# Performance work log

Measured on AMD Instinct MI355X. Metric: run time of the kernel, lower is better.

The kernel has to match this reference:

```python
import jax, jax.numpy as jnp
import numpy as np

HIDDEN = 1024
INNER = 2048  # hidden * expand_factor
STATE = 64
K = 4  # conv kernel size
BATCH, SEQ = 2, 2048


def setup_inputs() -> dict:
    key = jax.random.key(0)
    ks = jax.random.split(key, 8)
    def w(k, shape, scale=0.02):
        return (jax.random.normal(k, shape, jnp.float32) * scale)
    return {
        "x": jax.random.normal(ks[0], (BATCH, SEQ, HIDDEN), jnp.float32),
        "W_in": w(ks[1], (HIDDEN, 2 * INNER)),
        "conv_w": w(ks[2], (INNER, 1, K), 0.2),   # depthwise conv kernel [O, I/groups=1, K]
        "conv_b": jnp.zeros((INNER,), jnp.float32),
        "W_dt": w(ks[3], (INNER, INNER)),
        "b_dt": jnp.linspace(-4.0, -2.0, INNER).astype(jnp.float32),  # log(exp(linspace)) = linspace
        "W_B": w(ks[4], (INNER, STATE)),
        "W_C": w(ks[5], (INNER, STATE)),
        "D": jnp.ones((INNER,), jnp.float32),
        "W_out": w(ks[6], (INNER, HIDDEN)),
    }


def reference(x, W_in, conv_w, conv_b, W_dt, b_dt, W_B, W_C, D, W_out):
    batch, seq_len, _ = x.shape
    inner = W_dt.shape[0]
    state_dim = W_B.shape[1]

    # input projection and gate split
    xz = x @ W_in                              # [B, L, 2*inner]
    x_inner, z = jnp.split(xz, 2, axis=-1)

    # causal depthwise conv1d (pad both sides by K-1 then truncate == left-pad K-1)
    xc = jnp.transpose(x_inner, (0, 2, 1))    # [B, inner, L]
    k = conv_w.shape[-1]
    xc = jax.lax.conv_general_dilated(
        xc, conv_w, window_strides=(1,), padding=[(k - 1, 0)],
        dimension_numbers=("NCH", "OIH", "NCH"), feature_group_count=inner)
    xc = xc + conv_b[None, :, None]
    xc = jax.nn.silu(jnp.transpose(xc, (0, 2, 1)))   # [B, L, inner]

    # selective SSM parameters
    dt = jax.nn.softplus(xc @ W_dt + b_dt)    # [B, L, inner]
    Bm = xc @ W_B                             # [B, L, N]
    Cm = xc @ W_C                             # [B, L, N]
    a = jnp.exp(-dt)                          # [B, L, inner]
    dtx = dt * xc                             # [B, L, inner]

    # sequential selective scan over time: state[B, inner, N]
    def step(state, inp):
        a_t, dtx_t, b_t, c_t = inp
        state = a_t[..., None] * state + dtx_t[..., None] * b_t[:, None, :]
        y_t = jnp.einsum("bin,bn->bi", state, c_t)
        return state, y_t

    init = jnp.zeros((batch, inner, state_dim), x.dtype)
    xs = (jnp.swapaxes(a, 0, 1), jnp.swapaxes(dtx, 0, 1),
          jnp.swapaxes(Bm, 0, 1), jnp.swapaxes(Cm, 0, 1))
    _, ys = jax.lax.scan(step, init, xs)      # ys: [L, B, inner]
    y = jnp.swapaxes(ys, 0, 1) + D * xc       # skip connection

    y = y * jax.nn.silu(z)                    # output gate
    return y @ W_out                          # [B, L, hidden]
```

## Files before the change

### kernel.cpp

```cpp
#include <hip/hip_runtime.h>
#include <hip/hip_bf16.h>
#include <math.h>

#define BATCH  2
#define SEQ    2048
#define HID    1024
#define INNER  2048
#define NSTATE 64
#define NTOK   (BATCH * SEQ)
#define TCHUNK 64
#define NCHUNK (SEQ / TCHUNK)
#define NMID   (INNER + 2 * NSTATE)
#define LDH    1056
#define LDI    2080

typedef __bf16 bf16x8 __attribute__((ext_vector_type(8)));
typedef float  f32x4  __attribute__((ext_vector_type(4)));

typedef const __attribute__((address_space(1))) char* gas_ptr;
typedef __attribute__((address_space(3))) char*       las_ptr;

__device__ __forceinline__ void gload16(const void* g, void* l) {
  __builtin_amdgcn_global_load_lds((gas_ptr)g, (las_ptr)l, 16, 0, 0);
}

__device__ __forceinline__ unsigned short f2bf(float f) {
  __hip_bfloat16 h = __float2bfloat16(f);
  return __builtin_bit_cast(unsigned short, h);
}
__device__ __forceinline__ float bf2f(unsigned short u) {
  unsigned int x = ((unsigned int)u) << 16;
  return __builtin_bit_cast(float, x);
}

__global__ __launch_bounds__(256) void cvt_pad_kernel(
    const float* __restrict__ in, __hip_bfloat16* __restrict__ out, int n4) {
  int i = blockIdx.x * 256 + threadIdx.x;
  if (i >= n4) return;
  const int r = i >> 8;
  const int c = (i & 255) * 4;
  float4 v = *(const float4*)&in[(size_t)r * HID + c];
  ushort4 u;
  u.x = f2bf(v.x); u.y = f2bf(v.y); u.z = f2bf(v.z); u.w = f2bf(v.w);
  *(ushort4*)&out[(size_t)r * LDH + c] = u;
}

__global__ __launch_bounds__(256) void transpose_cvt_kernel(
    const float* __restrict__ in, __hip_bfloat16* __restrict__ out,
    int R, int C, int ostride) {
  __shared__ float tile[32][33];
  int tx = threadIdx.x & 31, ty = threadIdx.x >> 5;
  int c0 = blockIdx.x * 32, r0 = blockIdx.y * 32;
#pragma unroll
  for (int i = 0; i < 4; ++i)
    tile[ty + 8 * i][tx] = in[(size_t)(r0 + ty + 8 * i) * C + c0 + tx];
  __syncthreads();
#pragma unroll
  for (int i = 0; i < 4; ++i)
    out[(size_t)(c0 + ty + 8 * i) * ostride + r0 + tx] =
        __float2bfloat16(tile[tx][ty + 8 * i]);
}

template <int EPI>
__global__ __launch_bounds__(256, 4) void gemm_bt_kernel(
    const __hip_bfloat16* __restrict__ A, const __hip_bfloat16* __restrict__ Bt,
    int M, int N, int Klen, int ldk, int gridN, int nwg, int mnwg,
    float* __restrict__ Cout, int ldc, int ldo,
    __hip_bfloat16* __restrict__ o0, __hip_bfloat16* __restrict__ o1) {
  __shared__ __align__(16) __hip_bfloat16 As[128 * 64];
  __shared__ __align__(16) __hip_bfloat16 Bs[128 * 64];
  const int tid = threadIdx.x;
  const int lane = tid & 63;
  const int w = tid >> 6;
  const int wr = w >> 1, wc = w & 1;

  const int orig = blockIdx.x;
  const int q8 = nwg >> 3, r8 = nwg & 7;
  const int xcd = orig & 7, seq = orig >> 3;
  const int wg = (xcd < r8 ? xcd * (q8 + 1) : r8 * (q8 + 1) + (xcd - r8) * q8) + seq;
  const int kz = wg / mnwg;
  const int wgr = wg - kz * mnwg;
  const int m0 = (wgr / gridN) * 128;
  const int n0 = (wgr % gridN) * 128;

  const __hip_bfloat16* Ab = A + (size_t)kz * Klen;
  const __hip_bfloat16* Bb = Bt + (size_t)kz * Klen;

  f32x4 acc[4][4];
#pragma unroll
  for (int i = 0; i < 4; ++i)
#pragma unroll
    for (int j = 0; j < 4; ++j)
#pragma unroll
      for (int r2 = 0; r2 < 4; ++r2) acc[i][j][r2] = 0.f;

  const int g8row = lane >> 3;
  const int scol = ((lane & 7) ^ g8row) * 8;
  const __hip_bfloat16* Agp = Ab + (size_t)(m0 + w * 32 + g8row) * ldk + scol;
  const __hip_bfloat16* Bgp = Bb + (size_t)(n0 + w * 32 + g8row) * ldk + scol;
  __hip_bfloat16* lA = As + (w * 32) * 64;
  __hip_bfloat16* lB = Bs + (w * 32) * 64;

  const int lrow = lane & 15, lk = lane >> 4;
  const int arow0 = wr * 64 + lrow;
  const int brow0 = wc * 64 + lrow;

  const int nt = Klen >> 6;
  for (int t = 0; t < nt; ++t) {
    __syncthreads();
#pragma unroll
    for (int g = 0; g < 4; ++g) {
      gload16(Agp + (size_t)(g * 8) * ldk + t * 64, lA + (g * 8) * 64);
      gload16(Bgp + (size_t)(g * 8) * ldk + t * 64, lB + (g * 8) * 64);
    }
    __syncthreads();
#pragma unroll
    for (int ss = 0; ss < 2; ++ss) {
      bf16x8 af[4], bv[4];
#pragma unroll
      for (int i = 0; i < 4; ++i) {
        const int ra = arow0 + i * 16;
        af[i] = *(const bf16x8*)(As + ra * 64 + (((ss * 4 + lk) ^ (ra & 7)) * 8));
        const int rb = brow0 + i * 16;
        bv[i] = *(const bf16x8*)(Bs + rb * 64 + (((ss * 4 + lk) ^ (rb & 7)) * 8));
      }
#pragma unroll
      for (int i = 0; i < 4; ++i)
#pragma unroll
        for (int j = 0; j < 4; ++j)
          acc[i][j] = __builtin_amdgcn_mfma_f32_16x16x32_bf16(af[i], bv[j], acc[i][j], 0, 0, 0);
    }
  }

#pragma unroll
  for (int i = 0; i < 4; ++i) {
#pragma unroll
    for (int j = 0; j < 4; ++j) {
#pragma unroll
      for (int r2 = 0; r2 < 4; ++r2) {
        const int row = m0 + wr * 64 + i * 16 + lk * 4 + r2;
        const int col = n0 + wc * 64 + j * 16 + lrow;
        const float v = acc[i][j][r2];
        if constexpr (EPI == 0) {
          Cout[(size_t)kz * M * ldc + (size_t)row * ldc + col] = v;
        } else if constexpr (EPI == 1) {
          if (col < INNER) o0[(size_t)row * ldo + col] = __float2bfloat16(v);
          else             o1[(size_t)row * ldo + (col - INNER)] = __float2bfloat16(v);
        } else {
          o0[(size_t)kz * M * ldc + (size_t)row * ldc + col] = __float2bfloat16(v);
        }
      }
    }
  }
}

__global__ __launch_bounds__(256) void reduce4b_kernel(
    const __hip_bfloat16* __restrict__ P, float* __restrict__ out, int n4) {
  int i = blockIdx.x * 256 + threadIdx.x;
  if (i >= n4) return;
  float4 acc = make_float4(0.f, 0.f, 0.f, 0.f);
#pragma unroll
  for (int pp = 0; pp < 4; ++pp) {
    ushort4 u = ((const ushort4*)P)[(size_t)pp * n4 + i];
    acc.x += bf2f(u.x); acc.y += bf2f(u.y); acc.z += bf2f(u.z); acc.w += bf2f(u.w);
  }
  ((float4*)out)[i] = acc;
}

__global__ __launch_bounds__(256) void conv_silu_kernel(
    const __hip_bfloat16* __restrict__ xin, const float* __restrict__ cw,
    const float* __restrict__ cb, __hip_bfloat16* __restrict__ xch) {
  int idx = blockIdx.x * 256 + threadIdx.x;
  int cg = idx & 511;
  int tok = idx >> 9;
  int c = cg * 4;
  int l = tok & (SEQ - 1);
  float wv[4][4];
#pragma unroll
  for (int i = 0; i < 4; ++i) {
    float4 w = *(const float4*)&cw[(c + i) * 4];
    wv[i][0] = w.x; wv[i][1] = w.y; wv[i][2] = w.z; wv[i][3] = w.w;
  }
  float4 bias = *(const float4*)&cb[c];
  float r0 = bias.x, r1 = bias.y, r2 = bias.z, r3 = bias.w;
#pragma unroll
  for (int k = 0; k < 4; ++k) {
    const int d = 3 - k;
    if (l >= d) {
      ushort4 xv = *(const ushort4*)&xin[(size_t)(tok - d) * LDI + c];
      r0 = fmaf(bf2f(xv.x), wv[0][k], r0);
      r1 = fmaf(bf2f(xv.y), wv[1][k], r1);
      r2 = fmaf(bf2f(xv.z), wv[2][k], r2);
      r3 = fmaf(bf2f(xv.w), wv[3][k], r3);
    }
  }
  r0 = r0 / (1.f + __expf(-r0));
  r1 = r1 / (1.f + __expf(-r1));
  r2 = r2 / (1.f + __expf(-r2));
  r3 = r3 / (1.f + __expf(-r3));
  ushort4 u;
  u.x = f2bf(r0); u.y = f2bf(r1); u.z = f2bf(r2); u.w = f2bf(r3);
  *(ushort4*)&xch[(size_t)tok * LDI + c] = u;
}

__global__ __launch_bounds__(256) void cumv_kernel(
    const __hip_bfloat16* __restrict__ P, const float* __restrict__ bdt,
    const __hip_bfloat16* __restrict__ xch,
    unsigned short* __restrict__ cumA, unsigned int* __restrict__ wT) {
  __shared__ float dpre[64][68];
  __shared__ float xcs[64][68];
  const int bk = blockIdx.y;
  const int c0 = blockIdx.x * 64;
  const int b = bk >> 5, k = bk & 31;
  const size_t tokbase = (size_t)(b * SEQ + k * TCHUNK);
  const unsigned short* P0 = (const unsigned short*)P;
  const unsigned short* P1 = P0 + (size_t)NTOK * NMID;
  const unsigned short* XC = (const unsigned short*)xch;

  const int g = threadIdx.x & 15;
  const int r0 = threadIdx.x >> 4;
  const float4 bias4 = *(const float4*)&bdt[c0 + g * 4];
#pragma unroll
  for (int rr = 0; rr < 4; ++rr) {
    const int row = r0 + rr * 16;
    const size_t tok = tokbase + row;
    ushort4 u0 = *(const ushort4*)&P0[tok * NMID + c0 + g * 4];
    ushort4 u1 = *(const ushort4*)&P1[tok * NMID + c0 + g * 4];
    ushort4 ux = *(const ushort4*)&XC[tok * LDI + c0 + g * 4];
    float4 d = make_float4(bf2f(u0.x) + bf2f(u1.x) + bias4.x,
                           bf2f(u0.y) + bf2f(u1.y) + bias4.y,
                           bf2f(u0.z) + bf2f(u1.z) + bias4.z,
                           bf2f(u0.w) + bf2f(u1.w) + bias4.w);
    *(float4*)&dpre[row][g * 4] = d;
    *(float4*)&xcs[row][g * 4] = make_float4(bf2f(ux.x), bf2f(ux.y), bf2f(ux.z), bf2f(ux.w));
  }
  __syncthreads();

  const int cl = threadIdx.x >> 2, h = threadIdx.x & 3;
  const int c = c0 + cl;
  float dt[16], lc[16];
  float cum = 1.f;
#pragma unroll
  for (int j = 0; j < 16; ++j) {
    const int t = h * 16 + j;
    const float dp = dpre[t][cl];
    const float dtv = (dp > 15.f) ? dp : log1pf(__expf(dp));
    dt[j] = dtv;
    cum *= __expf(-dtv);
    lc[j] = cum;
  }
  const int lane = threadIdx.x & 63;
  const int gbase = lane & ~3;
  const float s0 = __shfl(cum, gbase + 0);
  const float s1 = __shfl(cum, gbase + 1);
  const float s2 = __shfl(cum, gbase + 2);
  float pre = 1.f;
  if (h > 0) pre *= s0;
  if (h > 1) pre *= s1;
  if (h > 2) pre *= s2;
  unsigned int wreg[8];
#pragma unroll
  for (int j = 0; j < 16; ++j) {
    const int t = h * 16 + j;
    const float cg = fmaxf(pre * lc[j], 1e-30f);
    cumA[(tokbase + t) * INNER + c] = f2bf(cg);
    const unsigned short wb = f2bf(dt[j] * xcs[t][cl] / cg);
    if (j & 1) wreg[j >> 1] |= ((unsigned int)wb) << 16;
    else       wreg[j >> 1] = (unsigned int)wb;
  }
  uint4* dst = (uint4*)(wT + ((size_t)bk * INNER + c) * 32 + h * 8);
  dst[0] = make_uint4(wreg[0], wreg[1], wreg[2], wreg[3]);
  dst[1] = make_uint4(wreg[4], wreg[5], wreg[6], wreg[7]);
}

__global__ __launch_bounds__(256) void chunkG_kernel(
    const __hip_bfloat16* __restrict__ P,
    __hip_bfloat16* __restrict__ Abuf, __hip_bfloat16* __restrict__ BtBuf) {
  __shared__ float Bsh[TCHUNK][NSTATE + 4];
  __shared__ float Csh[16][NSTATE + 4];
  const int blk = blockIdx.x;
  const int bk = blk >> 2, qt = blk & 3;
  const int b = bk >> 5, k = bk & 31;
  const int tid = threadIdx.x;
  const size_t tokbase = (size_t)(b * SEQ + k * TCHUNK);
  const unsigned short* P0 = (const unsigned short*)P;
  const unsigned short* P1 = (const unsigned short*)P + (size_t)NTOK * NMID;

  for (int i = tid; i < TCHUNK * 16; i += 256) {
    const int row = i >> 4, q = i & 15;
    const size_t off = (tokbase + row) * NMID + INNER + q * 4;
    ushort4 u0 = *(const ushort4*)&P0[off];
    ushort4 u1 = *(const ushort4*)&P1[off];
    *(float4*)&Bsh[row][q * 4] = make_float4(
        bf2f(u0.x) + bf2f(u1.x), bf2f(u0.y) + bf2f(u1.y),
        bf2f(u0.z) + bf2f(u1.z), bf2f(u0.w) + bf2f(u1.w));
  }
  for (int i = tid; i < 16 * 16; i += 256) {
    const int row = i >> 4, q = i & 15;
    const size_t off = (tokbase + qt * 16 + row) * NMID + INNER + NSTATE + q * 4;
    ushort4 u0 = *(const ushort4*)&P0[off];
    ushort4 u1 = *(const ushort4*)&P1[off];
    *(float4*)&Csh[row][q * 4] = make_float4(
        bf2f(u0.x) + bf2f(u1.x), bf2f(u0.y) + bf2f(u1.y),
        bf2f(u0.z) + bf2f(u1.z), bf2f(u0.w) + bf2f(u1.w));
  }
  __syncthreads();
  for (int e = tid; e < 16 * 64; e += 256) {
    const int tl = e >> 6, tau = e & 63;
    const int t = qt * 16 + tl;
    float g = 0.f;
    if (tau <= t) {
#pragma unroll
      for (int q = 0; q < 16; ++q) {
        const float4 cv = *(const float4*)&Csh[tl][q * 4];
        const float4 bv = *(const float4*)&Bsh[tau][q * 4];
        g += cv.x * bv.x + cv.y * bv.y + cv.z * bv.z + cv.w * bv.w;
      }
    }
    Abuf[((size_t)bk * 64 + t) * 128 + tau] = __float2bfloat16(g);
  }
  for (int e = tid; e < 16 * 64; e += 256) {
    const int n2l = e >> 6, r = e & 63;
    const int n2 = qt * 16 + n2l;
    BtBuf[((size_t)bk * 64 + n2) * 64 + r] = __float2bfloat16(Bsh[r][n2]);
    Abuf[((size_t)bk * 64 + n2) * 128 + 64 + r] = __float2bfloat16(Csh[n2l][r]);
  }
}

__global__ __launch_bounds__(256, 4) void sloc_gemm_kernel(
    const __hip_bfloat16* __restrict__ wT, const __hip_bfloat16* __restrict__ BtBuf,
    const unsigned short* __restrict__ cumA, unsigned short* __restrict__ S) {
  __shared__ __align__(16) __hip_bfloat16 As[128 * 64];
  __shared__ __align__(16) __hip_bfloat16 Bs[64 * 64];
  const int tid = threadIdx.x;
  const int lane = tid & 63;
  const int w = tid >> 6;
  const int bk = blockIdx.x >> 4;
  const int ct = blockIdx.x & 15;
  const int b = bk >> 5, k = bk & 31;
  const int c0 = ct * 128;

  const int g8row = lane >> 3;
  const int scol = ((lane & 7) ^ g8row) * 8;
  const __hip_bfloat16* Ag = wT + ((size_t)bk * INNER + c0 + w * 32 + g8row) * 64 + scol;
  const __hip_bfloat16* Bg = BtBuf + ((size_t)bk * 64 + w * 16 + g8row) * 64 + scol;
  __hip_bfloat16* lA = As + (w * 32) * 64;
  __hip_bfloat16* lB = Bs + (w * 16) * 64;
#pragma unroll
  for (int g = 0; g < 4; ++g) gload16(Ag + (size_t)(g * 8) * 64, lA + (g * 8) * 64);
#pragma unroll
  for (int g = 0; g < 2; ++g) gload16(Bg + (size_t)(g * 8) * 64, lB + (g * 8) * 64);
  __syncthreads();

  const int lrow = lane & 15, lk = lane >> 4;
  f32x4 acc[2][4];
#pragma unroll
  for (int i = 0; i < 2; ++i)
#pragma unroll
    for (int j = 0; j < 4; ++j)
#pragma unroll
      for (int r2 = 0; r2 < 4; ++r2) acc[i][j][r2] = 0.f;

#pragma unroll
  for (int ss = 0; ss < 2; ++ss) {
    bf16x8 af[2], bv[4];
#pragma unroll
    for (int i = 0; i < 2; ++i) {
      const int ra = w * 32 + i * 16 + lrow;
      af[i] = *(const bf16x8*)(As + ra * 64 + (((ss * 4 + lk) ^ (ra & 7)) * 8));
    }
#pragma unroll
    for (int j = 0; j < 4; ++j) {
      const int rb = j * 16 + lrow;
      bv[j] = *(const bf16x8*)(Bs + rb * 64 + (((ss * 4 + lk) ^ (rb & 7)) * 8));
    }
#pragma unroll
    for (int i = 0; i < 2; ++i)
#pragma unroll
      for (int j = 0; j < 4; ++j)
        acc[i][j] = __builtin_amdgcn_mfma_f32_16x16x32_bf16(af[i], bv[j], acc[i][j], 0, 0, 0);
  }

  const size_t tokT = (size_t)(b * SEQ + k * TCHUNK + 63);
#pragma unroll
  for (int i = 0; i < 2; ++i) {
#pragma unroll
    for (int j = 0; j < 4; ++j) {
#pragma unroll
      for (int r2 = 0; r2 < 4; ++r2) {
        const int c = c0 + w * 32 + i * 16 + lk * 4 + r2;
        const int n = j * 16 + lrow;
        const float sc = bf2f(cumA[tokT * INNER + c]);
        S[((size_t)bk * INNER + c) * 64 + n] = f2bf(acc[i][j][r2] * sc);
      }
    }
  }
}

__global__ __launch_bounds__(256) void scan_combine_kernel(
    unsigned short* __restrict__ S, const unsigned short* __restrict__ cumA) {
  const int idx = blockIdx.x * 256 + threadIdx.x;
  const int n = idx & 63;
  const int c = (idx >> 6) & (INNER - 1);
  const int b = idx >> 17;
  float s = 0.f;
  for (int k = 0; k < NCHUNK; ++k) {
    const size_t cs = (size_t)(b * NCHUNK + k) * INNER + c;
    const size_t off = cs * 64 + n;
    const float loc = bf2f(S[off]);
    S[off] = f2bf(s);
    const float ak = bf2f(cumA[((size_t)(b * SEQ + k * TCHUNK + 63)) * INNER + c]);
    s = fmaf(ak, s, loc);
  }
}

__global__ __launch_bounds__(256, 4) void ypre_gemm_kernel(
    const __hip_bfloat16* __restrict__ Abuf, const __hip_bfloat16* __restrict__ wT,
    const unsigned short* __restrict__ S, const unsigned short* __restrict__ cumA,
    const __hip_bfloat16* __restrict__ xch, const __hip_bfloat16* __restrict__ zbf,
    const float* __restrict__ Dv, __hip_bfloat16* __restrict__ ygated) {
  __shared__ __align__(16) __hip_bfloat16 Asm[64 * 128];
  __shared__ __align__(16) __hip_bfloat16 Bsm[128 * 128];
  const int tid = threadIdx.x;
  const int lane = tid & 63;
  const int w = tid >> 6;
  const int bk = blockIdx.x >> 4;
  const int ct = blockIdx.x & 15;
  const int b = bk >> 5, k = bk & 31;
  const int c0 = ct * 128;

  {
#pragma unroll
    for (int g = 0; g < 4; ++g) {
      const int base = w * 16 + g * 4;
      const int col16s = (lane & 15) ^ ((base + (lane >> 4)) & 7);
      const __hip_bfloat16* src =
          Abuf + ((size_t)bk * 64 + base + (lane >> 4)) * 128 + col16s * 8;
      gload16(src, (char*)Asm + base * 256);
    }
  }
  {
    const int row = tid & 127, part = tid >> 7;
    const int c = c0 + row;
    if (part == 0) {
      const uint4* src = (const uint4*)(wT + ((size_t)bk * INNER + c) * 64);
#pragma unroll
      for (int s2 = 0; s2 < 8; ++s2) {
        uint4 v = src[s2];
        *(uint4*)((char*)Bsm + row * 256 + (s2 ^ (row & 7)) * 16) = v;
      }
    } else {
      const uint4* srcS = (const uint4*)(S + ((size_t)bk * INNER + c) * 64);
#pragma unroll
      for (int s2 = 0; s2 < 8; ++s2) {
        uint4 v = srcS[s2];
        *(uint4*)((char*)Bsm + row * 256 + ((8 + s2) ^ (row & 7)) * 16) = v;
      }
    }
  }
  __syncthreads();

  const int lrow = lane & 15, lk = lane >> 4;
  f32x4 acc[8];
#pragma unroll
  for (int j = 0; j < 8; ++j)
#pragma unroll
    for (int r2 = 0; r2 < 4; ++r2) acc[j][r2] = 0.f;

  const int ra = w * 16 + lrow;
#pragma unroll
  for (int kk = 0; kk < 4; ++kk) {
    const int csa = (kk * 4 + lk) ^ (ra & 7);
    bf16x8 af = *(const bf16x8*)((const char*)Asm + ra * 256 + csa * 16);
#pragma unroll
    for (int j = 0; j < 8; ++j) {
      const int rb = j * 16 + lrow;
      const int csb = (kk * 4 + lk) ^ (rb & 7);
      bf16x8 bv = *(const bf16x8*)((const char*)Bsm + rb * 256 + csb * 16);
      acc[j] = __builtin_amdgcn_mfma_f32_16x16x32_bf16(af, bv, acc[j], 0, 0, 0);
    }
  }

  const size_t tokb = (size_t)(b * SEQ + k * TCHUNK);
#pragma unroll
  for (int j = 0; j < 8; ++j) {
#pragma unroll
    for (int r2 = 0; r2 < 4; ++r2) {
      const int t = w * 16 + lk * 4 + r2;
      const int c = c0 + j * 16 + lrow;
      const size_t tok = tokb + t;
      const float ca = bf2f(cumA[tok * INNER + c]);
      const float xc = bf2f(*(const unsigned short*)&xch[tok * LDI + c]);
      const float z = bf2f(*(const unsigned short*)&zbf[tok * LDI + c]);
      const float yt = ca * acc[j][r2] + Dv[c] * xc;
      const float g = z / (1.f + __expf(-z));
      *(unsigned short*)&ygated[tok * LDI + c] = f2bf(yt * g);
    }
  }
}

extern "C" void kernel_launch(void* const* d_in, const int* in_sizes, int n_in,
                              void* d_out, int out_size, void* d_ws, size_t ws_size,
                              hipStream_t stream) {
  const float* x      = (const float*)d_in[0];
  const float* W_in   = (const float*)d_in[1];
  const float* conv_w = (const float*)d_in[2];
  const float* conv_b = (const float*)d_in[3];
  const float* W_dt   = (const float*)d_in[4];
  const float* b_dt   = (const float*)d_in[5];
  const float* W_B    = (const float*)d_in[6];
  const float* W_C    = (const float*)d_in[7];
  const float* Dvec   = (const float*)d_in[8];
  const float* W_out  = (const float*)d_in[9];
  float* out = (float*)d_out;

  char* p = (char*)d_ws;
  auto alloc = [&](size_t bytes) {
    char* r = p;
    p += (bytes + 255) & ~(size_t)255;
    return r;
  };
  __hip_bfloat16* xin   = (__hip_bfloat16*)alloc((size_t)NTOK * LDI * 2);
  __hip_bfloat16* zbf   = (__hip_bfloat16*)alloc((size_t)NTOK * LDI * 2);
  char*           scr   = alloc((size_t)NTOK * LDH * 2 + (size_t)2 * INNER * LDH * 2);
  __hip_bfloat16* WmidT = (__hip_bfloat16*)alloc((size_t)NMID * LDI * 2);
  __hip_bfloat16* WoutT = (__hip_bfloat16*)alloc((size_t)HID * LDI * 2);
  unsigned short* cumA  = (unsigned short*)alloc((size_t)NTOK * INNER * 2);
  __hip_bfloat16* wT    = (__hip_bfloat16*)alloc((size_t)BATCH * NCHUNK * INNER * TCHUNK * 2);
  __hip_bfloat16* Abuf  = (__hip_bfloat16*)alloc((size_t)BATCH * NCHUNK * 64 * 128 * 2);
  __hip_bfloat16* BtBuf = (__hip_bfloat16*)alloc((size_t)BATCH * NCHUNK * 64 * 64 * 2);
  __hip_bfloat16* Pmid  = (__hip_bfloat16*)alloc((size_t)2 * NTOK * NMID * 2);

  __hip_bfloat16* x_bf   = (__hip_bfloat16*)scr;
  __hip_bfloat16* WinT   = (__hip_bfloat16*)(scr + (size_t)NTOK * LDH * 2);
  __hip_bfloat16* xch    = (__hip_bfloat16*)scr;
  __hip_bfloat16* ygated = xin;
  unsigned short* S      = (unsigned short*)Pmid;
  __hip_bfloat16* Pout   = Pmid;

  cvt_pad_kernel<<<(NTOK * HID / 4 + 255) / 256, 256, 0, stream>>>(x, x_bf, NTOK * HID / 4);
  transpose_cvt_kernel<<<dim3((2 * INNER) / 32, HID / 32), 256, 0, stream>>>(W_in, WinT, HID, 2 * INNER, LDH);
  transpose_cvt_kernel<<<dim3(INNER / 32, INNER / 32), 256, 0, stream>>>(W_dt, WmidT, INNER, INNER, LDI);
  transpose_cvt_kernel<<<dim3(NSTATE / 32, INNER / 32), 256, 0, stream>>>(
      W_B, WmidT + (size_t)INNER * LDI, INNER, NSTATE, LDI);
  transpose_cvt_kernel<<<dim3(NSTATE / 32, INNER / 32), 256, 0, stream>>>(
      W_C, WmidT + (size_t)(INNER + NSTATE) * LDI, INNER, NSTATE, LDI);
  transpose_cvt_kernel<<<dim3(HID / 32, INNER / 32), 256, 0, stream>>>(W_out, WoutT, INNER, HID, LDI);

  {
    const int gridN = (2 * INNER) / 128, nwg = (NTOK / 128) * gridN;
    gemm_bt_kernel<1><<<nwg, 256, 0, stream>>>(
        x_bf, WinT, NTOK, 2 * INNER, HID, LDH, gridN, nwg, nwg, nullptr, 0, LDI, xin, zbf);
  }

  conv_silu_kernel<<<(NTOK * (INNER / 4)) / 256, 256, 0, stream>>>(xin, conv_w, conv_b, xch);

  {
    const int gridN = NMID / 128;
    const int mnwg = (NTOK / 128) * gridN;
    const int nwg = mnwg * 2;
    gemm_bt_kernel<2><<<nwg, 256, 0, stream>>>(
        xch, WmidT, NTOK, NMID, INNER / 2, LDI, gridN, nwg, mnwg, nullptr, NMID, 0,
        Pmid, nullptr);
  }

  cumv_kernel<<<dim3(INNER / 64, BATCH * NCHUNK), 256, 0, stream>>>(
      Pmid, b_dt, xch, cumA, (unsigned int*)wT);
  chunkG_kernel<<<BATCH * NCHUNK * 4, 256, 0, stream>>>(Pmid, Abuf, BtBuf);
  sloc_gemm_kernel<<<BATCH * NCHUNK * 16, 256, 0, stream>>>(wT, BtBuf, cumA, S);
  scan_combine_kernel<<<(BATCH * INNER * NSTATE) / 256, 256, 0, stream>>>(S, cumA);
  ypre_gemm_kernel<<<BATCH * NCHUNK * 16, 256, 0, stream>>>(
      Abuf, wT, S, cumA, xch, zbf, Dvec, ygated);

  {
    const int gridN = HID / 128;
    const int mnwg = (NTOK / 128) * gridN;
    const int nwg = mnwg * 4;
    gemm_bt_kernel<2><<<nwg, 256, 0, stream>>>(
        ygated, WoutT, NTOK, HID, INNER / 4, LDI, gridN, nwg, mnwg, nullptr, HID, 0,
        Pout, nullptr);
    const int n4 = NTOK * HID / 4;
    reduce4b_kernel<<<(n4 + 255) / 256, 256, 0, stream>>>(Pout, out, n4);
  }
}
```

Measured before the change: 294.5 us.

## Store cumulative decay transposed per chunk and compute it via log-sum exp

The cumulative decay array moves from token-major [tok][channel] to a per-chunk channel-major [chunk][channel][t] layout matching wT. Its writes in cumv become packed 16-byte vector stores instead of scattered 2-byte stores, and its reads in sloc_gemm, scan_combine and ypre become contiguous. The decay is now computed as exp(-sum dt) with the sum clamped at 80, and the weight uses exp(+sum) in place of dividing by the product. This changes numerics slightly and replaces the earlier 1e-30 floor with the clamp.

```diff
diff --git a/kernel.cpp b/kernel.cpp
--- a/kernel.cpp
+++ b/kernel.cpp
@@ -206,7 +206,7 @@
 __global__ __launch_bounds__(256) void cumv_kernel(
     const __hip_bfloat16* __restrict__ P, const float* __restrict__ bdt,
     const __hip_bfloat16* __restrict__ xch,
-    unsigned short* __restrict__ cumA, unsigned int* __restrict__ wT) {
+    unsigned short* __restrict__ cumT, unsigned int* __restrict__ wT) {
   __shared__ float dpre[64][68];
   __shared__ float xcs[64][68];
   const int bk = blockIdx.y;
@@ -238,39 +238,49 @@
 
   const int cl = threadIdx.x >> 2, h = threadIdx.x & 3;
   const int c = c0 + cl;
-  float dt[16], lc[16];
-  float cum = 1.f;
+  float dt[16], ls[16];
+  float sdt = 0.f;
 #pragma unroll
   for (int j = 0; j < 16; ++j) {
     const int t = h * 16 + j;
     const float dp = dpre[t][cl];
     const float dtv = (dp > 15.f) ? dp : log1pf(__expf(dp));
     dt[j] = dtv;
-    cum *= __expf(-dtv);
-    lc[j] = cum;
+    sdt += dtv;
+    ls[j] = sdt;
   }
   const int lane = threadIdx.x & 63;
   const int gbase = lane & ~3;
-  const float s0 = __shfl(cum, gbase + 0);
-  const float s1 = __shfl(cum, gbase + 1);
-  const float s2 = __shfl(cum, gbase + 2);
-  float pre = 1.f;
-  if (h > 0) pre *= s0;
-  if (h > 1) pre *= s1;
-  if (h > 2) pre *= s2;
-  unsigned int wreg[8];
+  const float s0 = __shfl(sdt, gbase + 0);
+  const float s1 = __shfl(sdt, gbase + 1);
+  const float s2 = __shfl(sdt, gbase + 2);
+  float pre = 0.f;
+  if (h > 0) pre += s0;
+  if (h > 1) pre += s1;
+  if (h > 2) pre += s2;
+  unsigned int creg[8], wreg[8];
 #pragma unroll
   for (int j = 0; j < 16; ++j) {
     const int t = h * 16 + j;
-    const float cg = fmaxf(pre * lc[j], 1e-30f);
-    cumA[(tokbase + t) * INNER + c] = f2bf(cg);
-    const unsigned short wb = f2bf(dt[j] * xcs[t][cl] / cg);
-    if (j & 1) wreg[j >> 1] |= ((unsigned int)wb) << 16;
-    else       wreg[j >> 1] = (unsigned int)wb;
-  }
-  uint4* dst = (uint4*)(wT + ((size_t)bk * INNER + c) * 32 + h * 8);
-  dst[0] = make_uint4(wreg[0], wreg[1], wreg[2], wreg[3]);
-  dst[1] = make_uint4(wreg[4], wreg[5], wreg[6], wreg[7]);
+    const float st = fminf(pre + ls[j], 80.f);
+    const float cg = __expf(-st);
+    const float wi = __expf(st);
+    const unsigned short cb = f2bf(cg);
+    const unsigned short wb = f2bf(dt[j] * xcs[t][cl] * wi);
+    if (j & 1) {
+      creg[j >> 1] |= ((unsigned int)cb) << 16;
+      wreg[j >> 1] |= ((unsigned int)wb) << 16;
+    } else {
+      creg[j >> 1] = (unsigned int)cb;
+      wreg[j >> 1] = (unsigned int)wb;
+    }
+  }
+  uint4* cd = (uint4*)((unsigned int*)cumT + ((size_t)bk * INNER + c) * 32 + h * 8);
+  cd[0] = make_uint4(creg[0], creg[1], creg[2], creg[3]);
+  cd[1] = make_uint4(creg[4], creg[5], creg[6], creg[7]);
+  uint4* wd = (uint4*)(wT + ((size_t)bk * INNER + c) * 32 + h * 8);
+  wd[0] = make_uint4(wreg[0], wreg[1], wreg[2], wreg[3]);
+  wd[1] = make_uint4(wreg[4], wreg[5], wreg[6], wreg[7]);
 }
 
 __global__ __launch_bounds__(256) void chunkG_kernel(
@@ -329,7 +339,7 @@
 
 __global__ __launch_bounds__(256, 4) void sloc_gemm_kernel(
     const __hip_bfloat16* __restrict__ wT, const __hip_bfloat16* __restrict__ BtBuf,
-    const unsigned short* __restrict__ cumA, unsigned short* __restrict__ S) {
+    const unsigned short* __restrict__ cumT, unsigned short* __restrict__ S) {
   __shared__ __align__(16) __hip_bfloat16 As[128 * 64];
   __shared__ __align__(16) __hip_bfloat16 Bs[64 * 64];
   const int tid = threadIdx.x;
@@ -337,7 +347,6 @@
   const int w = tid >> 6;
   const int bk = blockIdx.x >> 4;
   const int ct = blockIdx.x & 15;
-  const int b = bk >> 5, k = bk & 31;
   const int c0 = ct * 128;
 
   const int g8row = lane >> 3;
@@ -381,7 +390,6 @@
         acc[i][j] = __builtin_amdgcn_mfma_f32_16x16x32_bf16(af[i], bv[j], acc[i][j], 0, 0, 0);
   }
 
-  const size_t tokT = (size_t)(b * SEQ + k * TCHUNK + 63);
 #pragma unroll
   for (int i = 0; i < 2; ++i) {
 #pragma unroll
@@ -390,7 +398,7 @@
       for (int r2 = 0; r2 < 4; ++r2) {
         const int c = c0 + w * 32 + i * 16 + lk * 4 + r2;
         const int n = j * 16 + lrow;
-        const float sc = bf2f(cumA[tokT * INNER + c]);
+        const float sc = bf2f(cumT[((size_t)bk * INNER + c) * 64 + 63]);
         S[((size_t)bk * INNER + c) * 64 + n] = f2bf(acc[i][j][r2] * sc);
       }
     }
@@ -398,7 +406,7 @@
 }
 
 __global__ __launch_bounds__(256) void scan_combine_kernel(
-    unsigned short* __restrict__ S, const unsigned short* __restrict__ cumA) {
+    unsigned short* __restrict__ S, const unsigned short* __restrict__ cumT) {
   const int idx = blockIdx.x * 256 + threadIdx.x;
   const int n = idx & 63;
   const int c = (idx >> 6) & (INNER - 1);
@@ -409,14 +417,14 @@
     const size_t off = cs * 64 + n;
     const float loc = bf2f(S[off]);
     S[off] = f2bf(s);
-    const float ak = bf2f(cumA[((size_t)(b * SEQ + k * TCHUNK + 63)) * INNER + c]);
+    const float ak = bf2f(cumT[cs * 64 + 63]);
     s = fmaf(ak, s, loc);
   }
 }
 
 __global__ __launch_bounds__(256, 4) void ypre_gemm_kernel(
     const __hip_bfloat16* __restrict__ Abuf, const __hip_bfloat16* __restrict__ wT,
-    const unsigned short* __restrict__ S, const unsigned short* __restrict__ cumA,
+    const unsigned short* __restrict__ S, const unsigned short* __restrict__ cumT,
     const __hip_bfloat16* __restrict__ xch, const __hip_bfloat16* __restrict__ zbf,
     const float* __restrict__ Dv, __hip_bfloat16* __restrict__ ygated) {
   __shared__ __align__(16) __hip_bfloat16 Asm[64 * 128];
@@ -484,12 +492,13 @@
   const size_t tokb = (size_t)(b * SEQ + k * TCHUNK);
 #pragma unroll
   for (int j = 0; j < 8; ++j) {
+    const int c = c0 + j * 16 + lrow;
+    const unsigned short* cp = cumT + ((size_t)bk * INNER + c) * 64 + w * 16 + lk * 4;
 #pragma unroll
     for (int r2 = 0; r2 < 4; ++r2) {
       const int t = w * 16 + lk * 4 + r2;
-      const int c = c0 + j * 16 + lrow;
       const size_t tok = tokb + t;
-      const float ca = bf2f(cumA[tok * INNER + c]);
+      const float ca = bf2f(cp[r2]);
       const float xc = bf2f(*(const unsigned short*)&xch[tok * LDI + c]);
       const float z = bf2f(*(const unsigned short*)&zbf[tok * LDI + c]);
       const float yt = ca * acc[j][r2] + Dv[c] * xc;
@@ -525,7 +534,7 @@
   char*           scr   = alloc((size_t)NTOK * LDH * 2 + (size_t)2 * INNER * LDH * 2);
   __hip_bfloat16* WmidT = (__hip_bfloat16*)alloc((size_t)NMID * LDI * 2);
   __hip_bfloat16* WoutT = (__hip_bfloat16*)alloc((size_t)HID * LDI * 2);
-  unsigned short* cumA  = (unsigned short*)alloc((size_t)NTOK * INNER * 2);
+  unsigned short* cumT  = (unsigned short*)alloc((size_t)BATCH * NCHUNK * INNER * TCHUNK * 2);
   __hip_bfloat16* wT    = (__hip_bfloat16*)alloc((size_t)BATCH * NCHUNK * INNER * TCHUNK * 2);
   __hip_bfloat16* Abuf  = (__hip_bfloat16*)alloc((size_t)BATCH * NCHUNK * 64 * 128 * 2);
   __hip_bfloat16* BtBuf = (__hip_bfloat16*)alloc((size_t)BATCH * NCHUNK * 64 * 64 * 2);
@@ -565,12 +574,12 @@
   }
 
   cumv_kernel<<<dim3(INNER / 64, BATCH * NCHUNK), 256, 0, stream>>>(
-      Pmid, b_dt, xch, cumA, (unsigned int*)wT);
+      Pmid, b_dt, xch, cumT, (unsigned int*)wT);
   chunkG_kernel<<<BATCH * NCHUNK * 4, 256, 0, stream>>>(Pmid, Abuf, BtBuf);
-  sloc_gemm_kernel<<<BATCH * NCHUNK * 16, 256, 0, stream>>>(wT, BtBuf, cumA, S);
-  scan_combine_kernel<<<(BATCH * INNER * NSTATE) / 256, 256, 0, stream>>>(S, cumA);
+  sloc_gemm_kernel<<<BATCH * NCHUNK * 16, 256, 0, stream>>>(wT, BtBuf, cumT, S);
+  scan_combine_kernel<<<(BATCH * INNER * NSTATE) / 256, 256, 0, stream>>>(S, cumT);
   ypre_gemm_kernel<<<BATCH * NCHUNK * 16, 256, 0, stream>>>(
-      Abuf, wT, S, cumA, xch, zbf, Dvec, ygated);
+      Abuf, wT, S, cumT, xch, zbf, Dvec, ygated);
 
   {
     const int gridN = HID / 128;
```

After: 285.9 us. 2.9% less time.
